# Kernel tuning notes

Hardware: AMD Instinct MI355X
Metric: run time of the kernel (lower is better)

Reference implementation:

```python
import jax, jax.numpy as jnp
import numpy as np

C = 512
H_HEADS = 8
HEAD_DIM = C // H_HEADS


def setup_inputs() -> dict:
    key = jax.random.key(0)
    ks = jax.random.split(key, 6)
    B, Hs, Ws = 16, 32, 32
    x = jax.random.normal(ks[0], (B, C, Hs, Ws), dtype=jnp.float32)
    qkv_w = jax.random.normal(ks[1], (3 * C, C), dtype=jnp.float32) * 0.02
    proj_w = jax.random.normal(ks[2], (C, C), dtype=jnp.float32) * 0.02
    proj_b = jnp.zeros((C,), dtype=jnp.float32)
    ln_g = jnp.ones((C,), dtype=jnp.float32)
    ln_b = jnp.zeros((C,), dtype=jnp.float32)
    return {"x": x, "qkv_w": qkv_w, "proj_w": proj_w, "proj_b": proj_b,
            "ln_g": ln_g, "ln_b": ln_b}


def _layernorm(x, g, b, eps=1e-5):
    mu = jnp.mean(x, axis=-1, keepdims=True)
    var = jnp.var(x, axis=-1, keepdims=True)
    return (x - mu) * jax.lax.rsqrt(var + eps) * g + b


def reference(x, qkv_w, proj_w, proj_b, ln_g, ln_b):
    B, Cc, Hs, Ws = x.shape
    N = Hs * Ws
    # (B, N, C)
    x_flat = x.reshape(B, Cc, N).transpose(0, 2, 1)
    x_norm = _layernorm(x_flat, ln_g, ln_b)
    # qkv: torch Linear y = x @ W^T
    qkv = x_norm @ qkv_w.T  # (B, N, 3C)
    qkv = qkv.reshape(B, N, 3, H_HEADS, HEAD_DIM).transpose(2, 0, 3, 1, 4)
    q, k, v = qkv[0], qkv[1], qkv[2]  # (B, h, N, d)
    scale = HEAD_DIM ** -0.5
    attn = jnp.einsum('bhnd,bhmd->bhnm', q, k) * scale
    attn = jax.nn.softmax(attn, axis=-1)
    out = jnp.einsum('bhnm,bhmd->bhnd', attn, v)  # (B, h, N, d)
    out = out.transpose(0, 2, 1, 3).reshape(B, N, Cc)
    out = out @ proj_w.T + proj_b
    out = out + x_flat
    return out.transpose(0, 2, 1).reshape(B, Cc, Hs, Ws)
```

## Files before the change

kernel.cpp:

```cpp
#include <hip/hip_runtime.h>
#include <stdint.h>

typedef unsigned short u16;
typedef __attribute__((ext_vector_type(4))) float f32x4;
typedef __attribute__((ext_vector_type(8))) short s16x8;
typedef __attribute__((ext_vector_type(4))) unsigned short u16x4;
typedef __attribute__((ext_vector_type(8))) unsigned short u16x8;
typedef __attribute__((ext_vector_type(4))) unsigned int u32x4;

__device__ __forceinline__ u16 f2bf(float f) {
  union { float f; uint32_t u; } v; v.f = f;
  uint32_t r = (v.u + 0x7FFFu + ((v.u >> 16) & 1u)) >> 16;
  return (u16)r;
}

__device__ __forceinline__ uint32_t cvtpk(float lo, float hi) {
  uint32_t r;
  asm("v_cvt_pk_bf16_f32 %0, %1, %2" : "=v"(r) : "v"(lo), "v"(hi));
  return r;
}

__device__ __forceinline__ float fexp2(float x) {
#if __has_builtin(__builtin_amdgcn_exp2f)
  return __builtin_amdgcn_exp2f(x);
#else
  float r; asm("v_exp_f32 %0, %1" : "=v"(r) : "v"(x)); return r;
#endif
}

__device__ __forceinline__ void gload_lds16(const void* g, void* l) {
  __builtin_amdgcn_global_load_lds((const __attribute__((address_space(1))) uint32_t*)g,
                                   (__attribute__((address_space(3))) uint32_t*)l, 16, 0, 0);
}

__global__ __launch_bounds__(256) void cvt_kernel(const float* __restrict__ src,
                                                  u16* __restrict__ dst, int n) {
  const int i = (blockIdx.x * 256 + threadIdx.x) * 4;
  if (i < n) {
    f32x4 v = *(const f32x4*)(src + i);
    u16x4 p;
    p[0] = f2bf(v[0]); p[1] = f2bf(v[1]); p[2] = f2bf(v[2]); p[3] = f2bf(v[3]);
    *(u16x4*)(dst + i) = p;
  }
}

__global__ __launch_bounds__(256) void ln_kernel(const float* __restrict__ x,
                                                 const float* __restrict__ lng,
                                                 const float* __restrict__ lnb,
                                                 u16* __restrict__ xn) {
  __shared__ float xt[16][516];
  __shared__ float ps[16][16], pq[16][16];
  __shared__ float smu[16], srs[16];
  const int tid = threadIdx.x;
  const int tok0 = blockIdx.x << 4;
  const int b = tok0 >> 10;
  const int nb = tok0 & 1023;
  const float* xb = x + (size_t)b * 512 * 1024 + nb;
  {
    const int n4 = (tid & 3) * 4;
    const int cr = tid >> 2;
#pragma unroll
    for (int it = 0; it < 8; ++it) {
      const int c = it * 64 + cr;
      f32x4 v = *(const f32x4*)(xb + (size_t)c * 1024 + n4);
      xt[n4 + 0][c] = v[0]; xt[n4 + 1][c] = v[1];
      xt[n4 + 2][c] = v[2]; xt[n4 + 3][c] = v[3];
    }
  }
  __syncthreads();
  {
    const int n = tid & 15, part = tid >> 4;
    float s = 0.f, q = 0.f;
#pragma unroll
    for (int i = 0; i < 8; ++i) {
      f32x4 v = *(const f32x4*)&xt[n][part * 32 + i * 4];
#pragma unroll
      for (int j = 0; j < 4; ++j) { s += v[j]; q += v[j] * v[j]; }
    }
    ps[part][n] = s; pq[part][n] = q;
  }
  __syncthreads();
  if (tid < 16) {
    float s = 0.f, q = 0.f;
#pragma unroll
    for (int p = 0; p < 16; ++p) { s += ps[p][tid]; q += pq[p][tid]; }
    const float mu = s * (1.f / 512.f);
    const float var = q * (1.f / 512.f) - mu * mu;
    smu[tid] = mu; srs[tid] = rsqrtf(var + 1e-5f);
  }
  __syncthreads();
  {
    const int n = tid >> 4, sub = tid & 15;
    const float mu = smu[n], rs = srs[n];
    u16* dst = xn + (size_t)(tok0 + n) * 512;
#pragma unroll
    for (int i = 0; i < 4; ++i) {
      const int c = (sub + 16 * i) * 8;
      f32x4 v0 = *(const f32x4*)&xt[n][c];
      f32x4 v1 = *(const f32x4*)&xt[n][c + 4];
      f32x4 g0 = *(const f32x4*)(lng + c);
      f32x4 g1 = *(const f32x4*)(lng + c + 4);
      f32x4 b0 = *(const f32x4*)(lnb + c);
      f32x4 b1 = *(const f32x4*)(lnb + c + 4);
      union { u32x4 w; u16x8 v; } pk;
      float r0 = (v0[0] - mu) * rs * g0[0] + b0[0];
      float r1 = (v0[1] - mu) * rs * g0[1] + b0[1];
      float r2 = (v0[2] - mu) * rs * g0[2] + b0[2];
      float r3 = (v0[3] - mu) * rs * g0[3] + b0[3];
      float r4 = (v1[0] - mu) * rs * g1[0] + b1[0];
      float r5 = (v1[1] - mu) * rs * g1[1] + b1[1];
      float r6 = (v1[2] - mu) * rs * g1[2] + b1[2];
      float r7 = (v1[3] - mu) * rs * g1[3] + b1[3];
      pk.w[0] = cvtpk(r0, r1); pk.w[1] = cvtpk(r2, r3);
      pk.w[2] = cvtpk(r4, r5); pk.w[3] = cvtpk(r6, r7);
      *(u16x8*)(dst + c) = pk.v;
    }
  }
}

template <int EPI>
__global__ __launch_bounds__(256) void gemm_bt(const u16* __restrict__ A,
                                               const u16* __restrict__ Bw,
                                               void* __restrict__ Cout,
                                               u16* __restrict__ vt,
                                               const float* __restrict__ bias,
                                               const float* __restrict__ resid,
                                               int M, int N, int K,
                                               long bsz, long csz, long rsz) {
  __shared__ union {
    struct { u16 A[2][128 * 32]; u16 B[2][128 * 32]; } m;
    u16 t[128 * 136];
  } sg;
  const int tid = threadIdx.x;
  const int w = tid >> 6, lane = tid & 63;
  const int lg = lane >> 4, l15 = lane & 15;
  const int wr = w >> 1, wc = w & 1;
  int m0, n0, z;
  if (EPI == 0) {
    const int blk = blockIdx.x;
    const int c = blk & 7, j = blk >> 3;
    m0 = (c * 16 + j / 12) * 128;
    n0 = (j % 12) * 128;
    z = 0;
  } else {
    m0 = blockIdx.x * 128; n0 = blockIdx.y * 128; z = blockIdx.z;
  }
  const u16* Bz = Bw + (size_t)z * bsz;
  const float* Rz = (EPI == 1) ? resid + (size_t)z * rsz : nullptr;

  f32x4 acc[4][4];
#pragma unroll
  for (int i = 0; i < 4; ++i)
#pragma unroll
    for (int j = 0; j < 4; ++j) acc[i][j] = (f32x4){0.f, 0.f, 0.f, 0.f};

  const int sr = lane >> 2, sch = (lane & 3) * 8;
  const u16* ap = A + (size_t)(m0 + w * 32 + sr) * K + sch;
  const u16* bp = Bz + (size_t)(n0 + w * 32 + sr) * K + sch;

  auto stage = [&](int buf) {
    gload_lds16(ap,          &sg.m.A[buf][(w * 32 + 0) * 32]);
    gload_lds16(ap + 16 * K, &sg.m.A[buf][(w * 32 + 16) * 32]);
    gload_lds16(bp,          &sg.m.B[buf][(w * 32 + 0) * 32]);
    gload_lds16(bp + 16 * K, &sg.m.B[buf][(w * 32 + 16) * 32]);
    ap += 32; bp += 32;
  };
  auto compute = [&](int buf) {
    s16x8 af[4], bfr[4];
#pragma unroll
    for (int mi = 0; mi < 4; ++mi)
      af[mi] = *(const s16x8*)&sg.m.A[buf][(wr * 64 + mi * 16 + l15) * 32 + lg * 8];
#pragma unroll
    for (int ni = 0; ni < 4; ++ni)
      bfr[ni] = *(const s16x8*)&sg.m.B[buf][(wc * 64 + ni * 16 + l15) * 32 + lg * 8];
#pragma unroll
    for (int mi = 0; mi < 4; ++mi)
#pragma unroll
      for (int ni = 0; ni < 4; ++ni)
        acc[mi][ni] = __builtin_amdgcn_mfma_f32_16x16x32_bf16(af[mi], bfr[ni], acc[mi][ni], 0, 0, 0);
  };

  const int nk2 = K >> 6;
  stage(0);
#pragma unroll 1
  for (int it = 0; it < nk2 - 1; ++it) {
    stage(1);
    asm volatile("s_waitcnt vmcnt(4)" ::: "memory");
    __builtin_amdgcn_s_barrier();
    asm volatile("" ::: "memory");
    compute(0);
    asm volatile("" ::: "memory");
    __builtin_amdgcn_s_barrier();
    stage(0);
    asm volatile("s_waitcnt vmcnt(4)" ::: "memory");
    __builtin_amdgcn_s_barrier();
    asm volatile("" ::: "memory");
    compute(1);
    asm volatile("" ::: "memory");
    __builtin_amdgcn_s_barrier();
  }
  stage(1);
  asm volatile("s_waitcnt vmcnt(4)" ::: "memory");
  __builtin_amdgcn_s_barrier();
  asm volatile("" ::: "memory");
  compute(0);
  asm volatile("" ::: "memory");
  __builtin_amdgcn_s_barrier();
  asm volatile("s_waitcnt vmcnt(0)" ::: "memory");
  __builtin_amdgcn_s_barrier();
  asm volatile("" ::: "memory");
  compute(1);

  if (EPI == 0) {
    u16* C = (u16*)Cout;
    if (n0 < 1024) {
      const float ce = (n0 < 512) ? 0.125f * 1.44269504f : 1.0f;
      __syncthreads();
#pragma unroll
      for (int mi = 0; mi < 4; ++mi)
#pragma unroll
        for (int ni = 0; ni < 4; ++ni) {
          const int colb = wc * 64 + ni * 16 + l15;
#pragma unroll
          for (int r = 0; r < 4; ++r) {
            const int rowb = wr * 64 + mi * 16 + lg * 4 + r;
            sg.t[rowb * 136 + colb] = (u16)cvtpk(acc[mi][ni][r] * ce, 0.f);
          }
        }
      __syncthreads();
#pragma unroll
      for (int itr = 0; itr < 8; ++itr) {
        const int rowb = itr * 16 + (tid >> 4);
        u16x8 v8 = *(const u16x8*)&sg.t[rowb * 136 + (tid & 15) * 8];
        *(u16x8*)(C + (size_t)(m0 + rowb) * 1024 + n0 + (tid & 15) * 8) = v8;
      }
    } else {
#pragma unroll
      for (int mi = 0; mi < 4; ++mi)
#pragma unroll
        for (int ni = 0; ni < 4; ++ni) {
          const int vcol = n0 - 1024 + wc * 64 + ni * 16 + l15;
          const int hh = vcol >> 6, d = vcol & 63;
          const int token = m0 + wr * 64 + mi * 16 + lg * 4;
          const int b = token >> 10, g15 = (token >> 6) & 15;
          const int p = 32 * (mi >> 1) + 8 * lg + 4 * (mi & 1);
          union { uint32_t w[2]; u16x4 v; } pk;
          pk.w[0] = cvtpk(acc[mi][ni][0], acc[mi][ni][1]);
          pk.w[1] = cvtpk(acc[mi][ni][2], acc[mi][ni][3]);
          *(u16x4*)&vt[(size_t)((b * 8 + hh) * 64 + d) * 1024 + g15 * 64 + p] = pk.v;
        }
    }
  } else {
    float* C = (float*)Cout + (size_t)z * csz;
#pragma unroll
    for (int mi = 0; mi < 4; ++mi)
#pragma unroll
      for (int ni = 0; ni < 4; ++ni) {
        const int col = n0 + wc * 64 + ni * 16 + l15;
#pragma unroll
        for (int r = 0; r < 4; ++r) {
          const int row = m0 + wr * 64 + mi * 16 + lg * 4 + r;
          C[(size_t)row * N + col] = acc[mi][ni][r] + bias[row] + Rz[(size_t)row * N + col];
        }
      }
  }
}

__global__ __launch_bounds__(256, 4) void attn_kernel(const u16* __restrict__ qk,
                                                      const u16* __restrict__ vt,
                                                      u16* __restrict__ ao) {
  __shared__ union {
    struct { u16 K[2][64 * 72]; u16 V[2][64 * 72]; } s;
    struct { float O[4][16][68]; float ls[4 * 32]; } e;
  } sm;
  const int tid = threadIdx.x;
  const int w = tid >> 6, lane = tid & 63;
  const int lg = lane >> 4, l15 = lane & 15;
  const int blk = blockIdx.x;
  const int qb = (blk >> 3) & 7;
  const int bh = (blk & 7) | ((blk >> 6) << 3);
  const int b = bh >> 3, h = bh & 7;
  const size_t qbase = (size_t)b * 1024 * 1024;
  const size_t vbase = (size_t)bh * 64 * 1024;
  const int qtok0 = qb * 128 + w * 32;

  s16x8 qf[2][2];
#pragma unroll
  for (int s = 0; s < 2; ++s)
#pragma unroll
    for (int qg = 0; qg < 2; ++qg)
      qf[s][qg] = *(const s16x8*)(qk + qbase + (size_t)(qtok0 + qg * 16 + l15) * 1024 +
                                  h * 64 + lg * 8 + 32 * s);

  f32x4 o[2][4];
  f32x4 lacc[2];
#pragma unroll
  for (int qg = 0; qg < 2; ++qg) {
    lacc[qg] = (f32x4){0.f, 0.f, 0.f, 0.f};
#pragma unroll
    for (int db = 0; db < 4; ++db) o[qg][db] = (f32x4){0.f, 0.f, 0.f, 0.f};
  }
  s16x8 ones;
#pragma unroll
  for (int j = 0; j < 8; ++j) ones[j] = (short)0x3F80;

  const int srr = lane >> 3, sch = lane & 7;
  const int row0 = w * 16 + srr;
  const u16* kp0 = qk + qbase + (size_t)row0 * 1024 + 512 + h * 64 + sch * 8;
  const u16* kp1 = kp0 + 8 * 1024;
  const u16* vp0 = vt + vbase + (size_t)row0 * 1024 + sch * 8;
  const u16* vp1 = vp0 + 8 * 1024;

  u32x4 kr0, kr1, vr0, vr1;
  auto loadr = [&]() {
    kr0 = *(const u32x4*)kp0; kr1 = *(const u32x4*)kp1;
    vr0 = *(const u32x4*)vp0; vr1 = *(const u32x4*)vp1;
    kp0 += 64 * 1024; kp1 += 64 * 1024;
    vp0 += 64; vp1 += 64;
  };
  const int woff0 = (w * 16 + srr) * 72 + sch * 8;
  const int woff1 = (w * 16 + 8 + srr) * 72 + sch * 8;
  auto writeb = [&](int buf) {
    *(u32x4*)&sm.s.K[buf][woff0] = kr0;
    *(u32x4*)&sm.s.K[buf][woff1] = kr1;
    *(u32x4*)&sm.s.V[buf][woff0] = vr0;
    *(u32x4*)&sm.s.V[buf][woff1] = vr1;
  };

  auto compute = [&](int buf) {
    f32x4 st[4][2];
#pragma unroll
    for (int kg = 0; kg < 4; ++kg)
#pragma unroll
      for (int qg = 0; qg < 2; ++qg) st[kg][qg] = (f32x4){0.f, 0.f, 0.f, 0.f};
    __builtin_amdgcn_s_setprio(1);
#pragma unroll
    for (int s = 0; s < 2; ++s)
#pragma unroll
      for (int kg = 0; kg < 4; ++kg) {
        const int row = kg * 16 + l15;
        s16x8 kf = *(const s16x8*)&sm.s.K[buf][row * 72 + lg * 8 + 32 * s];
#pragma unroll
        for (int qg = 0; qg < 2; ++qg)
          st[kg][qg] = __builtin_amdgcn_mfma_f32_16x16x32_bf16(kf, qf[s][qg], st[kg][qg], 0, 0, 0);
      }
    __builtin_amdgcn_s_setprio(0);

    s16x8 pa[2][2];
#pragma unroll
    for (int qg = 0; qg < 2; ++qg) {
      float pv[16];
#pragma unroll
      for (int kg = 0; kg < 4; ++kg)
#pragma unroll
        for (int r = 0; r < 4; ++r)
          pv[kg * 4 + r] = fexp2(st[kg][qg][r]);
#pragma unroll
      for (int kh = 0; kh < 2; ++kh) {
        union { u32x4 wd; s16x8 v; } pk;
        pk.wd[0] = cvtpk(pv[8 * kh + 0], pv[8 * kh + 1]);
        pk.wd[1] = cvtpk(pv[8 * kh + 2], pv[8 * kh + 3]);
        pk.wd[2] = cvtpk(pv[8 * kh + 4], pv[8 * kh + 5]);
        pk.wd[3] = cvtpk(pv[8 * kh + 6], pv[8 * kh + 7]);
        pa[qg][kh] = pk.v;
      }
    }

    __builtin_amdgcn_s_setprio(1);
#pragma unroll
    for (int kh = 0; kh < 2; ++kh) {
#pragma unroll
      for (int db = 0; db < 4; ++db) {
        const int d = db * 16 + l15;
        s16x8 vf = *(const s16x8*)&sm.s.V[buf][d * 72 + kh * 32 + lg * 8];
#pragma unroll
        for (int qg = 0; qg < 2; ++qg)
          o[qg][db] = __builtin_amdgcn_mfma_f32_16x16x32_bf16(pa[qg][kh], vf, o[qg][db], 0, 0, 0);
      }
#pragma unroll
      for (int qg = 0; qg < 2; ++qg)
        lacc[qg] = __builtin_amdgcn_mfma_f32_16x16x32_bf16(pa[qg][kh], ones, lacc[qg], 0, 0, 0);
    }
    __builtin_amdgcn_s_setprio(0);
  };

  loadr(); writeb(0);
  asm volatile("s_waitcnt lgkmcnt(0)" ::: "memory");
  __builtin_amdgcn_s_barrier();
  asm volatile("" ::: "memory");
#pragma unroll 1
  for (int it = 0; it < 7; ++it) {
    loadr();
    compute(0);
    writeb(1);
    asm volatile("s_waitcnt lgkmcnt(0)" ::: "memory");
    __builtin_amdgcn_s_barrier();
    asm volatile("" ::: "memory");
    loadr();
    compute(1);
    writeb(0);
    asm volatile("s_waitcnt lgkmcnt(0)" ::: "memory");
    __builtin_amdgcn_s_barrier();
    asm volatile("" ::: "memory");
  }
  loadr();
  compute(0);
  writeb(1);
  asm volatile("s_waitcnt lgkmcnt(0)" ::: "memory");
  __builtin_amdgcn_s_barrier();
  asm volatile("" ::: "memory");
  compute(1);

  __syncthreads();
  if (l15 == 0) {
#pragma unroll
    for (int qg = 0; qg < 2; ++qg)
#pragma unroll
      for (int r = 0; r < 4; ++r)
        sm.e.ls[w * 32 + qg * 16 + lg * 4 + r] = lacc[qg][r];
  }
#pragma unroll
  for (int half = 0; half < 2; ++half) {
#pragma unroll
    for (int db = 0; db < 4; ++db)
#pragma unroll
      for (int r = 0; r < 4; ++r)
        sm.e.O[w][lg * 4 + r][db * 16 + l15] = o[half][db][r];
    __syncthreads();
    {
      const int q = lane & 15, dh = lane >> 4;
      const float inv = 1.0f / sm.e.ls[w * 32 + half * 16 + q];
      u16* dst = ao + (size_t)(b * 1024 + qtok0 + half * 16 + q) * 512 + h * 64 + dh * 16;
      f32x4 v0 = *(const f32x4*)&sm.e.O[w][q][dh * 16 + 0];
      f32x4 v1 = *(const f32x4*)&sm.e.O[w][q][dh * 16 + 4];
      f32x4 v2 = *(const f32x4*)&sm.e.O[w][q][dh * 16 + 8];
      f32x4 v3 = *(const f32x4*)&sm.e.O[w][q][dh * 16 + 12];
      union { u32x4 wd; u16x8 v; } p0, p1;
      p0.wd[0] = cvtpk(v0[0] * inv, v0[1] * inv);
      p0.wd[1] = cvtpk(v0[2] * inv, v0[3] * inv);
      p0.wd[2] = cvtpk(v1[0] * inv, v1[1] * inv);
      p0.wd[3] = cvtpk(v1[2] * inv, v1[3] * inv);
      p1.wd[0] = cvtpk(v2[0] * inv, v2[1] * inv);
      p1.wd[1] = cvtpk(v2[2] * inv, v2[3] * inv);
      p1.wd[2] = cvtpk(v3[0] * inv, v3[1] * inv);
      p1.wd[3] = cvtpk(v3[2] * inv, v3[3] * inv);
      *(u16x8*)(dst + 0) = p0.v;
      *(u16x8*)(dst + 8) = p1.v;
    }
    __syncthreads();
  }
}

extern "C" void kernel_launch(void* const* d_in, const int* in_sizes, int n_in,
                              void* d_out, int out_size, void* d_ws, size_t ws_size,
                              hipStream_t stream) {
  const float* x      = (const float*)d_in[0];
  const float* qkv_w  = (const float*)d_in[1];
  const float* proj_w = (const float*)d_in[2];
  const float* proj_b = (const float*)d_in[3];
  const float* ln_g   = (const float*)d_in[4];
  const float* ln_b   = (const float*)d_in[5];
  float* out = (float*)d_out;

  char* ws = (char*)d_ws;
  u16* xn  = (u16*)ws;
  u16* qk  = (u16*)(ws + (size_t)16 * 1024 * 1024);
  u16* vt  = (u16*)(ws + (size_t)48 * 1024 * 1024);
  u16* ao  = (u16*)(ws + (size_t)64 * 1024 * 1024);
  u16* qw  = (u16*)(ws + (size_t)80 * 1024 * 1024);
  u16* pw  = qw + 1536 * 512;

  cvt_kernel<<<768, 256, 0, stream>>>(qkv_w, qw, 1536 * 512);
  cvt_kernel<<<256, 256, 0, stream>>>(proj_w, pw, 512 * 512);
  ln_kernel<<<1024, 256, 0, stream>>>(x, ln_g, ln_b, xn);
  gemm_bt<0><<<1536, 256, 0, stream>>>(xn, qw, qk, vt, nullptr, nullptr,
                                       16384, 1024, 512, 0, 0, 0);
  attn_kernel<<<1024, 256, 0, stream>>>(qk, vt, ao);
  gemm_bt<1><<<dim3(4, 8, 16), 256, 0, stream>>>(pw, ao, out, nullptr, proj_b, x,
                                                 512, 1024, 512,
                                                 (long)1024 * 512, (long)512 * 1024,
                                                 (long)512 * 1024);
}
```

Before: 232.6 us.

## Triple-buffer GEMM, direct-to-LDS swizzled attention staging, XCD-aware proj grid

The GEMM now uses three LDS buffers with all K-steps unrolled for K=512, so two tiles are in flight while one is computed. The attention kernel drops its register round-trip for K/V and issues direct global-to-LDS loads into an XOR-swizzled unpadded layout, with matching swizzled reads. The output projection switches from a 3D grid to a 1D grid that maps batches onto chiplet groups. The larger GEMM LDS footprint may lower occupancy, and the GEMM loop now assumes K=512.

```diff
diff --git a/kernel.cpp b/kernel.cpp
--- a/kernel.cpp
+++ b/kernel.cpp
@@ -128,7 +128,7 @@
                                                int M, int N, int K,
                                                long bsz, long csz, long rsz) {
   __shared__ union {
-    struct { u16 A[2][128 * 32]; u16 B[2][128 * 32]; } m;
+    struct { u16 A[3][128 * 32]; u16 B[3][128 * 32]; } m;
     u16 t[128 * 136];
   } sg;
   const int tid = threadIdx.x;
@@ -143,7 +143,12 @@
     n0 = (j % 12) * 128;
     z = 0;
   } else {
-    m0 = blockIdx.x * 128; n0 = blockIdx.y * 128; z = blockIdx.z;
+    const int blk = blockIdx.x;
+    const int c = blk & 7, j = blk >> 3;
+    z = c * 2 + (j >> 5);
+    const int mn = j & 31;
+    m0 = (mn >> 3) * 128;
+    n0 = (mn & 7) * 128;
   }
   const u16* Bz = Bw + (size_t)z * bsz;
   const float* Rz = (EPI == 1) ? resid + (size_t)z * rsz : nullptr;
@@ -180,10 +185,201 @@
         acc[mi][ni] = __builtin_amdgcn_mfma_f32_16x16x32_bf16(af[mi], bfr[ni], acc[mi][ni], 0, 0, 0);
   };
 
-  const int nk2 = K >> 6;
+  stage(0); stage(1); stage(2);
+#define GSTEP(BUF, NCNT, DOSTAGE)                                  \
+  asm volatile("s_waitcnt vmcnt(" #NCNT ")" ::: "memory");         \
+  __builtin_amdgcn_s_barrier();                                    \
+  asm volatile("" ::: "memory");                                   \
+  compute(BUF);                                                    \
+  asm volatile("" ::: "memory");                                   \
+  __builtin_amdgcn_s_barrier();                                    \
+  if (DOSTAGE) stage(BUF);
+#pragma unroll 1
+  for (int it = 0; it < 4; ++it) {
+    GSTEP(0, 8, 1)
+    GSTEP(1, 8, 1)
+    GSTEP(2, 8, 1)
+  }
+  GSTEP(0, 8, 1)
+  GSTEP(1, 8, 0)
+  GSTEP(2, 4, 0)
+  asm volatile("s_waitcnt vmcnt(0)" ::: "memory");
+  __builtin_amdgcn_s_barrier();
+  asm volatile("" ::: "memory");
+  compute(0);
+#undef GSTEP
+
+  if (EPI == 0) {
+    u16* C = (u16*)Cout;
+    if (n0 < 1024) {
+      const float ce = (n0 < 512) ? 0.125f * 1.44269504f : 1.0f;
+      __syncthreads();
+#pragma unroll
+      for (int mi = 0; mi < 4; ++mi)
+#pragma unroll
+        for (int ni = 0; ni < 4; ++ni) {
+          const int colb = wc * 64 + ni * 16 + l15;
+#pragma unroll
+          for (int r = 0; r < 4; ++r) {
+            const int rowb = wr * 64 + mi * 16 + lg * 4 + r;
+            sg.t[rowb * 136 + colb] = (u16)cvtpk(acc[mi][ni][r] * ce, 0.f);
+          }
+        }
+      __syncthreads();
+#pragma unroll
+      for (int itr = 0; itr < 8; ++itr) {
+        const int rowb = itr * 16 + (tid >> 4);
+        u16x8 v8 = *(const u16x8*)&sg.t[rowb * 136 + (tid & 15) * 8];
+        *(u16x8*)(C + (size_t)(m0 + rowb) * 1024 + n0 + (tid & 15) * 8) = v8;
+      }
+    } else {
+#pragma unroll
+      for (int mi = 0; mi < 4; ++mi)
+#pragma unroll
+        for (int ni = 0; ni < 4; ++ni) {
+          const int vcol = n0 - 1024 + wc * 64 + ni * 16 + l15;
+          const int hh = vcol >> 6, d = vcol & 63;
+          const int token = m0 + wr * 64 + mi * 16 + lg * 4;
+          const int b = token >> 10, g15 = (token >> 6) & 15;
+          const int p = 32 * (mi >> 1) + 8 * lg + 4 * (mi & 1);
+          union { uint32_t w[2]; u16x4 v; } pk;
+          pk.w[0] = cvtpk(acc[mi][ni][0], acc[mi][ni][1]);
+          pk.w[1] = cvtpk(acc[mi][ni][2], acc[mi][ni][3]);
+          *(u16x4*)&vt[(size_t)((b * 8 + hh) * 64 + d) * 1024 + g15 * 64 + p] = pk.v;
+        }
+    }
+  } else {
+    float* C = (float*)Cout + (size_t)z * csz;
+#pragma unroll
+    for (int mi = 0; mi < 4; ++mi)
+#pragma unroll
+      for (int ni = 0; ni < 4; ++ni) {
+        const int col = n0 + wc * 64 + ni * 16 + l15;
+#pragma unroll
+        for (int r = 0; r < 4; ++r) {
+          const int row = m0 + wr * 64 + mi * 16 + lg * 4 + r;
+          C[(size_t)row * N + col] = acc[mi][ni][r] + bias[row] + Rz[(size_t)row * N + col];
+        }
+      }
+  }
+}
+
+__global__ __launch_bounds__(256, 4) void attn_kernel(const u16* __restrict__ qk,
+                                                      const u16* __restrict__ vt,
+                                                      u16* __restrict__ ao) {
+  __shared__ union {
+    struct { u16 K[2][64 * 64]; u16 V[2][64 * 64]; } s;
+    struct { float O[4][16][68]; float ls[4 * 32]; } e;
+  } sm;
+  const int tid = threadIdx.x;
+  const int w = tid >> 6, lane = tid & 63;
+  const int lg = lane >> 4, l15 = lane & 15;
+  const int blk = blockIdx.x;
+  const int qb = (blk >> 3) & 7;
+  const int bh = (blk & 7) | ((blk >> 6) << 3);
+  const int b = bh >> 3, h = bh & 7;
+  const size_t qbase = (size_t)b * 1024 * 1024;
+  const size_t vbase = (size_t)bh * 64 * 1024;
+  const int qtok0 = qb * 128 + w * 32;
+
+  s16x8 qf[2][2];
+#pragma unroll
+  for (int s = 0; s < 2; ++s)
+#pragma unroll
+    for (int qg = 0; qg < 2; ++qg)
+      qf[s][qg] = *(const s16x8*)(qk + qbase + (size_t)(qtok0 + qg * 16 + l15) * 1024 +
+                                  h * 64 + lg * 8 + 32 * s);
+
+  f32x4 o[2][4];
+  f32x4 lacc[2];
+#pragma unroll
+  for (int qg = 0; qg < 2; ++qg) {
+    lacc[qg] = (f32x4){0.f, 0.f, 0.f, 0.f};
+#pragma unroll
+    for (int db = 0; db < 4; ++db) o[qg][db] = (f32x4){0.f, 0.f, 0.f, 0.f};
+  }
+  s16x8 ones;
+#pragma unroll
+  for (int j = 0; j < 8; ++j) ones[j] = (short)0x3F80;
+
+  const int srr = lane >> 3, sch = lane & 7;
+  const int row0 = w * 16 + srr, row1 = row0 + 8;
+  const u16* kp0 = qk + qbase + (size_t)row0 * 1024 + 512 + h * 64 + ((sch ^ (row0 & 7)) * 8);
+  const u16* kp1 = qk + qbase + (size_t)row1 * 1024 + 512 + h * 64 + ((sch ^ (row1 & 7)) * 8);
+  const u16* vp0 = vt + vbase + (size_t)row0 * 1024 + ((sch ^ (row0 & 7)) * 8);
+  const u16* vp1 = vt + vbase + (size_t)row1 * 1024 + ((sch ^ (row1 & 7)) * 8);
+
+  auto stage = [&](int buf) {
+    gload_lds16(kp0, &sm.s.K[buf][(w * 16 + 0) * 64]);
+    gload_lds16(kp1, &sm.s.K[buf][(w * 16 + 8) * 64]);
+    gload_lds16(vp0, &sm.s.V[buf][(w * 16 + 0) * 64]);
+    gload_lds16(vp1, &sm.s.V[buf][(w * 16 + 8) * 64]);
+    kp0 += 64 * 1024; kp1 += 64 * 1024;
+    vp0 += 64; vp1 += 64;
+  };
+
+  auto compute = [&](int buf) {
+    f32x4 st[4][2];
+#pragma unroll
+    for (int kg = 0; kg < 4; ++kg)
+#pragma unroll
+      for (int qg = 0; qg < 2; ++qg) st[kg][qg] = (f32x4){0.f, 0.f, 0.f, 0.f};
+    __builtin_amdgcn_s_setprio(1);
+#pragma unroll
+    for (int s = 0; s < 2; ++s)
+#pragma unroll
+      for (int kg = 0; kg < 4; ++kg) {
+        const int row = kg * 16 + l15;
+        s16x8 kf = *(const s16x8*)&sm.s.K[buf][row * 64 +
+                                              ((lg * 8 + 32 * s) ^ ((row & 7) << 3))];
+#pragma unroll
+        for (int qg = 0; qg < 2; ++qg)
+          st[kg][qg] = __builtin_amdgcn_mfma_f32_16x16x32_bf16(kf, qf[s][qg], st[kg][qg], 0, 0, 0);
+      }
+    __builtin_amdgcn_s_setprio(0);
+
+    s16x8 pa[2][2];
+#pragma unroll
+    for (int qg = 0; qg < 2; ++qg) {
+      float pv[16];
+#pragma unroll
+      for (int kg = 0; kg < 4; ++kg)
+#pragma unroll
+        for (int r = 0; r < 4; ++r)
+          pv[kg * 4 + r] = fexp2(st[kg][qg][r]);
+#pragma unroll
+      for (int kh = 0; kh < 2; ++kh) {
+        union { u32x4 wd; s16x8 v; } pk;
+        pk.wd[0] = cvtpk(pv[8 * kh + 0], pv[8 * kh + 1]);
+        pk.wd[1] = cvtpk(pv[8 * kh + 2], pv[8 * kh + 3]);
+        pk.wd[2] = cvtpk(pv[8 * kh + 4], pv[8 * kh + 5]);
+        pk.wd[3] = cvtpk(pv[8 * kh + 6], pv[8 * kh + 7]);
+        pa[qg][kh] = pk.v;
+      }
+    }
+
+    __builtin_amdgcn_s_setprio(1);
+#pragma unroll
+    for (int kh = 0; kh < 2; ++kh) {
+#pragma unroll
+      for (int db = 0; db < 4; ++db) {
+        const int d = db * 16 + l15;
+        s16x8 vf = *(const s16x8*)&sm.s.V[buf][d * 64 +
+                                               ((kh * 32 + lg * 8) ^ ((d & 7) << 3))];
+#pragma unroll
+        for (int qg = 0; qg < 2; ++qg)
+          o[qg][db] = __builtin_amdgcn_mfma_f32_16x16x32_bf16(pa[qg][kh], vf, o[qg][db], 0, 0, 0);
+      }
+#pragma unroll
+      for (int qg = 0; qg < 2; ++qg)
+        lacc[qg] = __builtin_amdgcn_mfma_f32_16x16x32_bf16(pa[qg][kh], ones, lacc[qg], 0, 0, 0);
+    }
+    __builtin_amdgcn_s_setprio(0);
+  };
+
   stage(0);
 #pragma unroll 1
-  for (int it = 0; it < nk2 - 1; ++it) {
+  for (int it = 0; it < 7; ++it) {
     stage(1);
     asm volatile("s_waitcnt vmcnt(4)" ::: "memory");
     __builtin_amdgcn_s_barrier();
@@ -207,206 +403,6 @@
   asm volatile("" ::: "memory");
   __builtin_amdgcn_s_barrier();
   asm volatile("s_waitcnt vmcnt(0)" ::: "memory");
-  __builtin_amdgcn_s_barrier();
-  asm volatile("" ::: "memory");
-  compute(1);
-
-  if (EPI == 0) {
-    u16* C = (u16*)Cout;
-    if (n0 < 1024) {
-      const float ce = (n0 < 512) ? 0.125f * 1.44269504f : 1.0f;
-      __syncthreads();
-#pragma unroll
-      for (int mi = 0; mi < 4; ++mi)
-#pragma unroll
-        for (int ni = 0; ni < 4; ++ni) {
-          const int colb = wc * 64 + ni * 16 + l15;
-#pragma unroll
-          for (int r = 0; r < 4; ++r) {
-            const int rowb = wr * 64 + mi * 16 + lg * 4 + r;
-            sg.t[rowb * 136 + colb] = (u16)cvtpk(acc[mi][ni][r] * ce, 0.f);
-          }
-        }
-      __syncthreads();
-#pragma unroll
-      for (int itr = 0; itr < 8; ++itr) {
-        const int rowb = itr * 16 + (tid >> 4);
-        u16x8 v8 = *(const u16x8*)&sg.t[rowb * 136 + (tid & 15) * 8];
-        *(u16x8*)(C + (size_t)(m0 + rowb) * 1024 + n0 + (tid & 15) * 8) = v8;
-      }
-    } else {
-#pragma unroll
-      for (int mi = 0; mi < 4; ++mi)
-#pragma unroll
-        for (int ni = 0; ni < 4; ++ni) {
-          const int vcol = n0 - 1024 + wc * 64 + ni * 16 + l15;
-          const int hh = vcol >> 6, d = vcol & 63;
-          const int token = m0 + wr * 64 + mi * 16 + lg * 4;
-          const int b = token >> 10, g15 = (token >> 6) & 15;
-          const int p = 32 * (mi >> 1) + 8 * lg + 4 * (mi & 1);
-          union { uint32_t w[2]; u16x4 v; } pk;
-          pk.w[0] = cvtpk(acc[mi][ni][0], acc[mi][ni][1]);
-          pk.w[1] = cvtpk(acc[mi][ni][2], acc[mi][ni][3]);
-          *(u16x4*)&vt[(size_t)((b * 8 + hh) * 64 + d) * 1024 + g15 * 64 + p] = pk.v;
-        }
-    }
-  } else {
-    float* C = (float*)Cout + (size_t)z * csz;
-#pragma unroll
-    for (int mi = 0; mi < 4; ++mi)
-#pragma unroll
-      for (int ni = 0; ni < 4; ++ni) {
-        const int col = n0 + wc * 64 + ni * 16 + l15;
-#pragma unroll
-        for (int r = 0; r < 4; ++r) {
-          const int row = m0 + wr * 64 + mi * 16 + lg * 4 + r;
-          C[(size_t)row * N + col] = acc[mi][ni][r] + bias[row] + Rz[(size_t)row * N + col];
-        }
-      }
-  }
-}
-
-__global__ __launch_bounds__(256, 4) void attn_kernel(const u16* __restrict__ qk,
-                                                      const u16* __restrict__ vt,
-                                                      u16* __restrict__ ao) {
-  __shared__ union {
-    struct { u16 K[2][64 * 72]; u16 V[2][64 * 72]; } s;
-    struct { float O[4][16][68]; float ls[4 * 32]; } e;
-  } sm;
-  const int tid = threadIdx.x;
-  const int w = tid >> 6, lane = tid & 63;
-  const int lg = lane >> 4, l15 = lane & 15;
-  const int blk = blockIdx.x;
-  const int qb = (blk >> 3) & 7;
-  const int bh = (blk & 7) | ((blk >> 6) << 3);
-  const int b = bh >> 3, h = bh & 7;
-  const size_t qbase = (size_t)b * 1024 * 1024;
-  const size_t vbase = (size_t)bh * 64 * 1024;
-  const int qtok0 = qb * 128 + w * 32;
-
-  s16x8 qf[2][2];
-#pragma unroll
-  for (int s = 0; s < 2; ++s)
-#pragma unroll
-    for (int qg = 0; qg < 2; ++qg)
-      qf[s][qg] = *(const s16x8*)(qk + qbase + (size_t)(qtok0 + qg * 16 + l15) * 1024 +
-                                  h * 64 + lg * 8 + 32 * s);
-
-  f32x4 o[2][4];
-  f32x4 lacc[2];
-#pragma unroll
-  for (int qg = 0; qg < 2; ++qg) {
-    lacc[qg] = (f32x4){0.f, 0.f, 0.f, 0.f};
-#pragma unroll
-    for (int db = 0; db < 4; ++db) o[qg][db] = (f32x4){0.f, 0.f, 0.f, 0.f};
-  }
-  s16x8 ones;
-#pragma unroll
-  for (int j = 0; j < 8; ++j) ones[j] = (short)0x3F80;
-
-  const int srr = lane >> 3, sch = lane & 7;
-  const int row0 = w * 16 + srr;
-  const u16* kp0 = qk + qbase + (size_t)row0 * 1024 + 512 + h * 64 + sch * 8;
-  const u16* kp1 = kp0 + 8 * 1024;
-  const u16* vp0 = vt + vbase + (size_t)row0 * 1024 + sch * 8;
-  const u16* vp1 = vp0 + 8 * 1024;
-
-  u32x4 kr0, kr1, vr0, vr1;
-  auto loadr = [&]() {
-    kr0 = *(const u32x4*)kp0; kr1 = *(const u32x4*)kp1;
-    vr0 = *(const u32x4*)vp0; vr1 = *(const u32x4*)vp1;
-    kp0 += 64 * 1024; kp1 += 64 * 1024;
-    vp0 += 64; vp1 += 64;
-  };
-  const int woff0 = (w * 16 + srr) * 72 + sch * 8;
-  const int woff1 = (w * 16 + 8 + srr) * 72 + sch * 8;
-  auto writeb = [&](int buf) {
-    *(u32x4*)&sm.s.K[buf][woff0] = kr0;
-    *(u32x4*)&sm.s.K[buf][woff1] = kr1;
-    *(u32x4*)&sm.s.V[buf][woff0] = vr0;
-    *(u32x4*)&sm.s.V[buf][woff1] = vr1;
-  };
-
-  auto compute = [&](int buf) {
-    f32x4 st[4][2];
-#pragma unroll
-    for (int kg = 0; kg < 4; ++kg)
-#pragma unroll
-      for (int qg = 0; qg < 2; ++qg) st[kg][qg] = (f32x4){0.f, 0.f, 0.f, 0.f};
-    __builtin_amdgcn_s_setprio(1);
-#pragma unroll
-    for (int s = 0; s < 2; ++s)
-#pragma unroll
-      for (int kg = 0; kg < 4; ++kg) {
-        const int row = kg * 16 + l15;
-        s16x8 kf = *(const s16x8*)&sm.s.K[buf][row * 72 + lg * 8 + 32 * s];
-#pragma unroll
-        for (int qg = 0; qg < 2; ++qg)
-          st[kg][qg] = __builtin_amdgcn_mfma_f32_16x16x32_bf16(kf, qf[s][qg], st[kg][qg], 0, 0, 0);
-      }
-    __builtin_amdgcn_s_setprio(0);
-
-    s16x8 pa[2][2];
-#pragma unroll
-    for (int qg = 0; qg < 2; ++qg) {
-      float pv[16];
-#pragma unroll
-      for (int kg = 0; kg < 4; ++kg)
-#pragma unroll
-        for (int r = 0; r < 4; ++r)
-          pv[kg * 4 + r] = fexp2(st[kg][qg][r]);
-#pragma unroll
-      for (int kh = 0; kh < 2; ++kh) {
-        union { u32x4 wd; s16x8 v; } pk;
-        pk.wd[0] = cvtpk(pv[8 * kh + 0], pv[8 * kh + 1]);
-        pk.wd[1] = cvtpk(pv[8 * kh + 2], pv[8 * kh + 3]);
-        pk.wd[2] = cvtpk(pv[8 * kh + 4], pv[8 * kh + 5]);
-        pk.wd[3] = cvtpk(pv[8 * kh + 6], pv[8 * kh + 7]);
-        pa[qg][kh] = pk.v;
-      }
-    }
-
-    __builtin_amdgcn_s_setprio(1);
-#pragma unroll
-    for (int kh = 0; kh < 2; ++kh) {
-#pragma unroll
-      for (int db = 0; db < 4; ++db) {
-        const int d = db * 16 + l15;
-        s16x8 vf = *(const s16x8*)&sm.s.V[buf][d * 72 + kh * 32 + lg * 8];
-#pragma unroll
-        for (int qg = 0; qg < 2; ++qg)
-          o[qg][db] = __builtin_amdgcn_mfma_f32_16x16x32_bf16(pa[qg][kh], vf, o[qg][db], 0, 0, 0);
-      }
-#pragma unroll
-      for (int qg = 0; qg < 2; ++qg)
-        lacc[qg] = __builtin_amdgcn_mfma_f32_16x16x32_bf16(pa[qg][kh], ones, lacc[qg], 0, 0, 0);
-    }
-    __builtin_amdgcn_s_setprio(0);
-  };
-
-  loadr(); writeb(0);
-  asm volatile("s_waitcnt lgkmcnt(0)" ::: "memory");
-  __builtin_amdgcn_s_barrier();
-  asm volatile("" ::: "memory");
-#pragma unroll 1
-  for (int it = 0; it < 7; ++it) {
-    loadr();
-    compute(0);
-    writeb(1);
-    asm volatile("s_waitcnt lgkmcnt(0)" ::: "memory");
-    __builtin_amdgcn_s_barrier();
-    asm volatile("" ::: "memory");
-    loadr();
-    compute(1);
-    writeb(0);
-    asm volatile("s_waitcnt lgkmcnt(0)" ::: "memory");
-    __builtin_amdgcn_s_barrier();
-    asm volatile("" ::: "memory");
-  }
-  loadr();
-  compute(0);
-  writeb(1);
-  asm volatile("s_waitcnt lgkmcnt(0)" ::: "memory");
   __builtin_amdgcn_s_barrier();
   asm volatile("" ::: "memory");
   compute(1);
@@ -476,8 +472,8 @@
   gemm_bt<0><<<1536, 256, 0, stream>>>(xn, qw, qk, vt, nullptr, nullptr,
                                        16384, 1024, 512, 0, 0, 0);
   attn_kernel<<<1024, 256, 0, stream>>>(qk, vt, ao);
-  gemm_bt<1><<<dim3(4, 8, 16), 256, 0, stream>>>(pw, ao, out, nullptr, proj_b, x,
-                                                 512, 1024, 512,
-                                                 (long)1024 * 512, (long)512 * 1024,
-                                                 (long)512 * 1024);
-}
+  gemm_bt<1><<<512, 256, 0, stream>>>(pw, ao, out, nullptr, proj_b, x,
+                                      512, 1024, 512,
+                                      (long)1024 * 512, (long)512 * 1024,
+                                      (long)512 * 1024);
+}
```

Result: faster. 218.7 us (-6.0%).
